# Kernel optimization log

Measured on AMD Instinct MI355X. Metric: run time of the kernel, lower is better.

Reference implementation:

```python
import jax, jax.numpy as jnp
import numpy as np
import jax.scipy.linalg as jsl

# ---- module constants (mirror __init__ buffers) ----
T0, T1, DT = 0.0, 1.0, 1e-3
DIM, NSTEPS, M, TQ, B = 8, 2048, 64, 1024, 1
DS = (T1 - T0) / NSTEPS
STEPS = jnp.linspace(T0, T1, NSTEPS + 1)            # [S+1]
ZPTS = jnp.linspace(T0 + DT * 5.5, T1 - DT * 5.5, M)  # inducing points [M]
SQRT_DS = float(np.sqrt(DS))
SQRT_DT = float(np.sqrt(DT))


def _hurst(t, y0, W1, b1, W2, b2, Wc1, bc1, Wc2, bc2, dw, cw):
    # compute_hurst: sigmoid(driving_action(t)*dw + condition_net(y0)*cw)
    tc_in = t.reshape(-1, 1)                                             # [N,1]
    feat = jnp.concatenate([jnp.sin(tc_in), jnp.cos(tc_in), tc_in], -1)  # [N,3]
    tc = jax.nn.sigmoid(jnp.tanh(feat @ W1.T + b1) @ W2.T + b2)          # [N,dim]
    pc = jax.nn.sigmoid(jnp.tanh(y0 @ Wc1.T + bc1) @ Wc2.T + bc2)        # [1,dim]
    return jax.nn.sigmoid(tc * dw + pc * cw)                             # [N,dim]


def _safe_pow(x, a):
    # x**a for x>=0, with well-defined (zero) gradient at x==0
    mask = x > 0
    xs = jnp.where(mask, x, 1.0)
    return jnp.where(mask, xs ** a, 0.0)


def _compute_weight(t, y0, params, eps=1e-12):
    # compute_weight (Muniandy et al. weight); returns [S, N, dim]
    h = _hurst(t, y0, *params)[None]                              # [1,N,dim]
    d0 = jax.nn.relu(t[None, :] - STEPS[:-1, None])[..., None]    # [S,N,1]
    d1 = jax.nn.relu(t[None, :] - STEPS[1:, None])[..., None]     # [S,N,1]
    w = jnp.sqrt(_safe_pow(d0, 2.0 * h) - _safe_pow(d1, 2.0 * h) + eps)
    w = w / jnp.sqrt(2.0 * h * DS)
    return w / jnp.exp(jax.lax.lgamma(h + 0.5))


def _increment_weight(t, y0, params):
    # increment_weight: g_i / dt (finite difference of clamped weights)
    wa = jnp.maximum(_compute_weight(t, y0, params), 0.0)
    wb = jnp.maximum(_compute_weight(t + DT, y0, params), 0.0)
    return jnp.maximum((wb - wa) * SQRT_DS / DT, 0.0)             # [S,N,dim]


def _forward(t, y0, eps_z, W1, b1, W2, b2, Wc1, bc1, Wc2, bc2, dw, cw):
    params = (W1, b1, W2, b2, Wc1, bc1, Wc2, bc2, dw, cw)
    # --- precompute (inducing points) ---
    Kz = _increment_weight(ZPTS, y0, params)                # [S,M,dim]
    Kzz = jnp.einsum('smd,skd->dmk', Kz, Kz)                # [dim,M,M]
    Lz = jnp.linalg.cholesky(Kzz + 1e-6 * jnp.eye(M, dtype=Kzz.dtype))
    delta_Bz = jnp.einsum('dmk,dkb->dmb', Lz, eps_z)        # [dim,M,B]
    # --- forward (mean / sqrt(var)*sqrt(dt)) ---
    Kt = _increment_weight(t, y0, params)                   # [S,T,dim]
    Ktz = jnp.einsum('std,smd->dtm', Kt, Kz)                # [dim,T,M]
    alpha = jax.vmap(lambda L, b: jsl.cho_solve((L, True), b))(
        Lz, jnp.swapaxes(Ktz, -1, -2))                      # [dim,M,T]
    mean = jnp.einsum('dmt,dmb->dtb', alpha, delta_Bz)      # [dim,T,B]
    Ktt = jnp.einsum('std,sud->dtu', Kt, Kt)                # [dim,T,T]
    var = Ktt - jnp.einsum('dmt,dmu->dtu', alpha, alpha)    # [dim,T,T]
    std = jnp.sqrt(jnp.maximum(var, 1e-12)) * SQRT_DT
    return mean.reshape(-1, DIM), std.reshape(-1, DIM)


def setup_inputs() -> dict:
    key = jax.random.key(0)
    ks = jax.random.split(key, 12)
    return {
        't': jax.random.uniform(ks[0], (TQ,), jnp.float32, T0 + 0.05, T1 - 0.05),
        'y0': jax.random.normal(ks[1], (1, 1), jnp.float32),
        'eps_z': jax.random.normal(ks[2], (DIM, M, B), jnp.float32),
        'W1': jax.random.normal(ks[3], (10, 3), jnp.float32) * 0.3,
        'b1': jax.random.normal(ks[4], (10,), jnp.float32) * 0.1,
        'W2': jax.random.normal(ks[5], (DIM, 10), jnp.float32) * 0.3,
        'b2': jax.random.normal(ks[6], (DIM,), jnp.float32) * 0.1,
        'Wc1': jax.random.normal(ks[7], (10, 1), jnp.float32) * 0.3,
        'bc1': jax.random.normal(ks[8], (10,), jnp.float32) * 0.1,
        'Wc2': jax.random.normal(ks[9], (DIM, 10), jnp.float32) * 0.3,
        'bc2': jax.random.normal(ks[10], (DIM,), jnp.float32) * 0.1,
        'dw': jnp.array([0.5], jnp.float32),
        'cw': jnp.array([0.5], jnp.float32),
    }


def reference(t, y0, eps_z, W1, b1, W2, b2, Wc1, bc1, Wc2, bc2, dw, cw):
    return _forward(t, y0, eps_z, W1, b1, W2, b2, Wc1, bc1, Wc2, bc2, dw, cw)
```

## Files before the change

### kernel.cpp

```cpp
#include <hip/hip_runtime.h>
#include <cmath>

#define DIMN 8
#define SSTEPS 2048
#define MZ 64
#define TQN 1024
#define DS_F    4.8828125e-4f
#define DT_F    1.0e-3f
#define SCALE_F 22.09708691207961f
#define SQRTDT_F 0.031622776601683794f
#define LN2_F   0.6931471805599453f

typedef _Float16 f16x8 __attribute__((ext_vector_type(8)));
typedef float f32x4 __attribute__((ext_vector_type(4)));

__device__ __forceinline__ float sigmoidf_(float x) { return 1.f / (1.f + expf(-x)); }

__device__ __forceinline__ void gl_lds16(const _Float16* g, _Float16* l)
{
    __builtin_amdgcn_global_load_lds(
        (const __attribute__((address_space(1))) unsigned int*)g,
        (__attribute__((address_space(3))) unsigned int*)l, 16, 0, 0);
}

__global__ void coef_kernel(const float* __restrict__ t_in, const float* __restrict__ y0,
                            const float* __restrict__ W1, const float* __restrict__ b1,
                            const float* __restrict__ W2, const float* __restrict__ b2,
                            const float* __restrict__ Wc1, const float* __restrict__ bc1,
                            const float* __restrict__ Wc2, const float* __restrict__ bc2,
                            const float* __restrict__ dw, const float* __restrict__ cw,
                            float4* __restrict__ coef_t, float4* __restrict__ coef_z,
                            float* __restrict__ times_z)
{
    int gid = blockIdx.x * blockDim.x + threadIdx.x;
    if (gid >= TQN + MZ) return;
    bool isz = gid >= TQN;
    float tv;
    if (!isz) {
        tv = t_in[gid];
    } else {
        int j = gid - TQN;
        tv = 0.0055f + (float)j * (0.989f / 63.0f);
        times_z[j] = tv;
    }
    float y = y0[0];
    float hc[10];
    #pragma unroll
    for (int j = 0; j < 10; ++j) hc[j] = tanhf(y * Wc1[j] + bc1[j]);
    float pc[DIMN];
    #pragma unroll
    for (int d = 0; d < DIMN; ++d) {
        float s = bc2[d];
        #pragma unroll
        for (int j = 0; j < 10; ++j) s += hc[j] * Wc2[d * 10 + j];
        pc[d] = sigmoidf_(s);
    }
    float dww = dw[0], cww = cw[0];
    float4 outv[DIMN];
    for (int which = 0; which < 2; ++which) {
        float tt = (which == 0) ? tv : tv + DT_F;
        float st = sinf(tt), ct = cosf(tt);
        float hid[10];
        #pragma unroll
        for (int j = 0; j < 10; ++j)
            hid[j] = tanhf(st * W1[j * 3 + 0] + ct * W1[j * 3 + 1] + tt * W1[j * 3 + 2] + b1[j]);
        #pragma unroll
        for (int d = 0; d < DIMN; ++d) {
            float s = b2[d];
            #pragma unroll
            for (int j = 0; j < 10; ++j) s += hid[j] * W2[d * 10 + j];
            float tc = sigmoidf_(s);
            float h = sigmoidf_(tc * dww + pc[d] * cww);
            float e = 2.f * h;
            float c = rsqrtf(e * DS_F) / tgammaf(h + 0.5f);
            if (which == 0) { outv[d].x = e; outv[d].y = c; }
            else            { outv[d].z = e; outv[d].w = c; }
        }
    }
    float4* dst = isz ? (coef_z + (size_t)(gid - TQN) * DIMN) : (coef_t + (size_t)gid * DIMN);
    #pragma unroll
    for (int d = 0; d < DIMN; ++d) dst[d] = outv[d];
}

__global__ __launch_bounds__(512) void sort_kernel(const float* __restrict__ t_in,
                                                   float* __restrict__ tsort,
                                                   int* __restrict__ perm,
                                                   int* __restrict__ inv)
{
    __shared__ float v[1024];
    __shared__ int   ix[1024];
    int tid = threadIdx.x;
    v[tid] = t_in[tid];             ix[tid] = tid;
    v[tid + 512] = t_in[tid + 512]; ix[tid + 512] = tid + 512;
    __syncthreads();
    for (int k = 2; k <= 1024; k <<= 1) {
        for (int j = k >> 1; j > 0; j >>= 1) {
            #pragma unroll 1
            for (int base = 0; base < 1024; base += 512) {
                int i = base + tid;
                int p = i ^ j;
                if (p > i) {
                    bool up = ((i & k) == 0);
                    float vi = v[i], vp = v[p];
                    if ((vi > vp) == up) {
                        v[i] = vp; v[p] = vi;
                        int q_ = ix[i]; ix[i] = ix[p]; ix[p] = q_;
                    }
                }
            }
            __syncthreads();
        }
    }
    tsort[tid] = v[tid];           tsort[tid + 512] = v[tid + 512];
    perm[tid] = ix[tid];           perm[tid + 512] = ix[tid + 512];
    inv[ix[tid]] = tid;            inv[ix[tid + 512]] = tid + 512;
}

__device__ __forceinline__ void side_weights(float tt, float e, float c, int sbase,
                                             float (&w)[8])
{
    float xprev = tt - (float)sbase * DS_F;
    float pa = 0.f;
    if (xprev > 0.f) pa = __builtin_amdgcn_exp2f(e * __builtin_amdgcn_logf(xprev));
    #pragma unroll
    for (int k = 1; k <= 8; ++k) {
        float xk = tt - (float)(sbase + k) * DS_F;
        float D, pan;
        if (xk > 0.f) {
            float om = xk * __builtin_amdgcn_rcpf(xprev);
            float y2 = e * __builtin_amdgcn_logf(om);
            float wl = y2 * LN2_F;
            float em = wl * (1.f + wl * (0.5f + wl * (0.16666667f + wl * (0.041666668f + wl * 0.008333334f))));
            float g = -em;
            if (wl < -0.3f) g = 1.f - __builtin_amdgcn_exp2f(y2);
            D = pa * g;
            pan = pa - D;
        } else {
            D = pa;
            pan = 0.f;
        }
        w[k - 1] = __builtin_amdgcn_sqrtf(D + 1e-12f) * c;
        pa = pan;
        xprev = xk;
    }
}

__device__ __forceinline__ unsigned pack_hl(float v)
{
    _Float16 h = (_Float16)v;
    _Float16 l = (_Float16)(v - (float)h);
    unsigned short hu = __builtin_bit_cast(unsigned short, h);
    unsigned short lu = __builtin_bit_cast(unsigned short, l);
    return (unsigned)hu | ((unsigned)lu << 16);
}

__global__ __launch_bounds__(256) void kmat_t_kernel(const float* __restrict__ tsort,
                                                     const int* __restrict__ perm,
                                                     const float4* __restrict__ coef,
                                                     _Float16* __restrict__ KThi,
                                                     _Float16* __restrict__ KTlo)
{
    int band = blockIdx.x >> 2;
    float bmax = tsort[band * 128 + 127];
    if ((float)(blockIdx.y * 64) * DS_F > bmax + DT_F + 0.07f) return;
    int tid = threadIdx.x;
    int txx = tid & 31, sidx = tid >> 5;
    int t = blockIdx.x * 32 + txx;
    int sbase = blockIdx.y * 64 + sidx * 8;
    int d = blockIdx.z;
    __shared__ unsigned shhl[32][65];
    float tq = tsort[t];
    float4 cf = coef[(size_t)perm[t] * DIMN + d];
    float wa[8], wb[8];
    side_weights(tq,        cf.x, cf.y, sbase, wa);
    side_weights(tq + DT_F, cf.z, cf.w, sbase, wb);
    #pragma unroll
    for (int k = 0; k < 8; ++k) {
        float v = fmaxf(wb[k] - wa[k], 0.f) * SCALE_F;
        shhl[txx][sidx * 8 + k] = pack_hl(v);
    }
    __syncthreads();
    int tl = tid >> 3, sc = tid & 7;
    unsigned dwv[8];
    #pragma unroll
    for (int j = 0; j < 8; ++j) dwv[j] = shhl[tl][sc * 8 + j];
    uint4 hv, lv;
    hv.x = __builtin_amdgcn_perm(dwv[1], dwv[0], 0x05040100u);
    hv.y = __builtin_amdgcn_perm(dwv[3], dwv[2], 0x05040100u);
    hv.z = __builtin_amdgcn_perm(dwv[5], dwv[4], 0x05040100u);
    hv.w = __builtin_amdgcn_perm(dwv[7], dwv[6], 0x05040100u);
    lv.x = __builtin_amdgcn_perm(dwv[1], dwv[0], 0x07060302u);
    lv.y = __builtin_amdgcn_perm(dwv[3], dwv[2], 0x07060302u);
    lv.z = __builtin_amdgcn_perm(dwv[5], dwv[4], 0x07060302u);
    lv.w = __builtin_amdgcn_perm(dwv[7], dwv[6], 0x07060302u);
    size_t o = ((size_t)(d * 1024) + blockIdx.x * 32 + tl) * 2048 + blockIdx.y * 64 + sc * 8;
    *(uint4*)&KThi[o] = hv;
    *(uint4*)&KTlo[o] = lv;
}

__global__ __launch_bounds__(256) void kmat_z_kernel(const float* __restrict__ times,
                                                     const float4* __restrict__ coef,
                                                     float* __restrict__ Kz,
                                                     _Float16* __restrict__ KzThi,
                                                     _Float16* __restrict__ KzTlo)
{
    int tid = threadIdx.x;
    int txx = tid & 31, sidx = tid >> 5;
    int m = blockIdx.x * 32 + txx;
    int sbase = blockIdx.y * 64 + sidx * 8;
    int d = blockIdx.z;
    __shared__ unsigned shhl[32][65];
    float tq = times[m];
    float4 cf = coef[(size_t)m * DIMN + d];
    float wa[8], wb[8];
    side_weights(tq,        cf.x, cf.y, sbase, wa);
    side_weights(tq + DT_F, cf.z, cf.w, sbase, wb);
    #pragma unroll
    for (int k = 0; k < 8; ++k) {
        float v = fmaxf(wb[k] - wa[k], 0.f) * SCALE_F;
        Kz[((size_t)d * SSTEPS + sbase + k) * 64 + m] = v;
        shhl[txx][sidx * 8 + k] = pack_hl(v);
    }
    __syncthreads();
    int tl = tid >> 3, sc = tid & 7;
    unsigned dwv[8];
    #pragma unroll
    for (int j = 0; j < 8; ++j) dwv[j] = shhl[tl][sc * 8 + j];
    uint4 hv, lv;
    hv.x = __builtin_amdgcn_perm(dwv[1], dwv[0], 0x05040100u);
    hv.y = __builtin_amdgcn_perm(dwv[3], dwv[2], 0x05040100u);
    hv.z = __builtin_amdgcn_perm(dwv[5], dwv[4], 0x05040100u);
    hv.w = __builtin_amdgcn_perm(dwv[7], dwv[6], 0x05040100u);
    lv.x = __builtin_amdgcn_perm(dwv[1], dwv[0], 0x07060302u);
    lv.y = __builtin_amdgcn_perm(dwv[3], dwv[2], 0x07060302u);
    lv.z = __builtin_amdgcn_perm(dwv[5], dwv[4], 0x07060302u);
    lv.w = __builtin_amdgcn_perm(dwv[7], dwv[6], 0x07060302u);
    size_t o = ((size_t)(d * 64) + blockIdx.x * 32 + tl) * 2048 + blockIdx.y * 64 + sc * 8;
    *(uint4*)&KzThi[o] = hv;
    *(uint4*)&KzTlo[o] = lv;
}

__global__ __launch_bounds__(256) void kzz_partial_kernel(const float* __restrict__ Kz,
                                                          float* __restrict__ part)
{
    int kidx = blockIdx.x;
    int d = blockIdx.y;
    int tid = threadIdx.x, tx = tid & 15, ty = tid >> 4;
    __shared__ float As[32][64];
    float acc[4][4] = {};
    const float* base = Kz + ((size_t)d * SSTEPS + (size_t)kidx * 256) * 64;
    for (int c = 0; c < 8; ++c) {
        __syncthreads();
        #pragma unroll
        for (int l = 0; l < 2; ++l) {
            int idx = tid + l * 256;
            int r = idx >> 4, c4 = idx & 15;
            *(float4*)&As[r][c4 * 4] = *(const float4*)(base + (size_t)(c * 32 + r) * 64 + c4 * 4);
        }
        __syncthreads();
        #pragma unroll
        for (int k = 0; k < 32; ++k) {
            float av[4], bv[4];
            *(float4*)&av[0] = *(float4*)&As[k][ty * 4];
            *(float4*)&bv[0] = *(float4*)&As[k][tx * 4];
            #pragma unroll
            for (int i = 0; i < 4; ++i)
                #pragma unroll
                for (int j = 0; j < 4; ++j) acc[i][j] += av[i] * bv[j];
        }
    }
    float* dst = part + (size_t)(kidx * DIMN + d) * 4096;
    #pragma unroll
    for (int i = 0; i < 4; ++i)
        *(float4*)&dst[(size_t)(ty * 4 + i) * 64 + tx * 4] =
            make_float4(acc[i][0], acc[i][1], acc[i][2], acc[i][3]);
}

__global__ void reduce_kernel(const float* __restrict__ in, float* __restrict__ out,
                              int n, int parts)
{
    int i = blockIdx.x * 256 + threadIdx.x;
    if (i >= n) return;
    float s = 0.f;
    for (int p = 0; p < parts; ++p) s += in[(size_t)p * n + i];
    out[i] = s;
}

__global__ __launch_bounds__(64) void chol_kernel(const float* __restrict__ Kzz,
                                                  const float* __restrict__ eps_z,
                                                  float* __restrict__ Lz, float* __restrict__ dBz)
{
    int d = blockIdx.x, i = threadIdx.x;
    __shared__ float A[64][65];
    for (int r = 0; r < 64; ++r)
        A[r][i] = Kzz[(size_t)d * 4096 + (size_t)r * 64 + i] + ((r == i) ? 1e-6f : 0.f);
    __syncthreads();
    for (int j = 0; j < 64; ++j) {
        float s = 0.f;
        if (i >= j) {
            float s0 = 0.f, s1 = 0.f, s2 = 0.f, s3 = 0.f;
            int k = 0;
            for (; k + 4 <= j; k += 4) {
                s0 += A[i][k]     * A[j][k];
                s1 += A[i][k + 1] * A[j][k + 1];
                s2 += A[i][k + 2] * A[j][k + 2];
                s3 += A[i][k + 3] * A[j][k + 3];
            }
            for (; k < j; ++k) s0 += A[i][k] * A[j][k];
            s = A[i][j] - ((s0 + s1) + (s2 + s3));
        }
        __syncthreads();
        if (i == j) A[j][j] = sqrtf(fmaxf(s, 1e-30f));
        __syncthreads();
        if (i > j) A[i][j] = s / A[j][j];
        __syncthreads();
    }
    for (int r = 0; r < 64; ++r)
        Lz[(size_t)d * 4096 + (size_t)r * 64 + i] = (i <= r) ? A[r][i] : 0.f;
    {
        float s0 = 0.f, s1 = 0.f, s2 = 0.f, s3 = 0.f;
        int k = 0;
        for (; k + 4 <= i + 1; k += 4) {
            s0 += A[i][k]     * eps_z[d * 64 + k];
            s1 += A[i][k + 1] * eps_z[d * 64 + k + 1];
            s2 += A[i][k + 2] * eps_z[d * 64 + k + 2];
            s3 += A[i][k + 3] * eps_z[d * 64 + k + 3];
        }
        for (; k <= i; ++k) s0 += A[i][k] * eps_z[d * 64 + k];
        dBz[d * 64 + i] = (s0 + s1) + (s2 + s3);
    }
}

__global__ __launch_bounds__(256, 2) void ktz_mfma_kernel(const _Float16* __restrict__ KThi,
                                                          const _Float16* __restrict__ KTlo,
                                                          const _Float16* __restrict__ KzThi,
                                                          const _Float16* __restrict__ KzTlo,
                                                          const float* __restrict__ tsort,
                                                          float* __restrict__ part)
{
    int tid = threadIdx.x;
    int wave = tid >> 6, lane = tid & 63;
    int n = lane & 15, q = lane >> 4;
    int lr = lane >> 2, lc = (lane & 3) * 8;
    int d = blockIdx.x;
    int t0 = blockIdx.y * 128;
    int split = blockIdx.z;
    int wr = (wave >> 1) * 64, wc = (wave & 1) * 32;

    float tmax = tsort[t0 + 127];
    int klim = (int)floorf((tmax + DT_F) * 64.f) + 2;
    int nc = klim - split * 16;
    nc = nc < 0 ? 0 : (nc > 16 ? 16 : nc);

    __shared__ _Float16 Ah[2][128][32], Al[2][128][32];
    __shared__ _Float16 Bh[2][64][32],  Bl[2][64][32];

    f32x4 acc[4][2];
    #pragma unroll
    for (int i = 0; i < 4; ++i)
        #pragma unroll
        for (int j = 0; j < 2; ++j) acc[i][j] = (f32x4)0.f;

    const size_t aRow = (size_t)(d * 1024 + t0);
    const size_t bRow = (size_t)(d * 64);
    int segA = wave * 32;
    int segB = wave * 16;

    auto stage = [&](int buf, int c) {
        int s0 = split * 512 + c * 32;
        size_t ga = (aRow + segA + lr) * 2048 + s0 + lc;
        size_t gb = (bRow + segB + lr) * 2048 + s0 + lc;
        gl_lds16(KThi + ga,               &Ah[buf][segA][0]);
        gl_lds16(KThi + ga + 16 * 2048,   &Ah[buf][segA + 16][0]);
        gl_lds16(KTlo + ga,               &Al[buf][segA][0]);
        gl_lds16(KTlo + ga + 16 * 2048,   &Al[buf][segA + 16][0]);
        gl_lds16(KzThi + gb,              &Bh[buf][segB][0]);
        gl_lds16(KzTlo + gb,              &Bl[buf][segB][0]);
    };

    if (nc > 0) stage(0, 0);
    for (int c = 0; c < nc; ++c) {
        int buf = c & 1;
        asm volatile("s_waitcnt vmcnt(0)" ::: "memory");
        __builtin_amdgcn_s_barrier();
        __builtin_amdgcn_sched_barrier(0);
        if (c + 1 < nc) stage(buf ^ 1, c + 1);
        f16x8 fAh[4], fAl[4], fBh[2], fBl[2];
        #pragma unroll
        for (int i = 0; i < 4; ++i) {
            fAh[i] = *(f16x8*)&Ah[buf][wr + i * 16 + n][q * 8];
            fAl[i] = *(f16x8*)&Al[buf][wr + i * 16 + n][q * 8];
        }
        #pragma unroll
        for (int j = 0; j < 2; ++j) {
            fBh[j] = *(f16x8*)&Bh[buf][wc + j * 16 + n][q * 8];
            fBl[j] = *(f16x8*)&Bl[buf][wc + j * 16 + n][q * 8];
        }
        __builtin_amdgcn_s_setprio(1);
        #pragma unroll
        for (int i = 0; i < 4; ++i)
            #pragma unroll
            for (int j = 0; j < 2; ++j) {
                acc[i][j] = __builtin_amdgcn_mfma_f32_16x16x32_f16(fAh[i], fBh[j], acc[i][j], 0, 0, 0);
                acc[i][j] = __builtin_amdgcn_mfma_f32_16x16x32_f16(fAh[i], fBl[j], acc[i][j], 0, 0, 0);
                acc[i][j] = __builtin_amdgcn_mfma_f32_16x16x32_f16(fAl[i], fBh[j], acc[i][j], 0, 0, 0);
            }
        __builtin_amdgcn_s_setprio(0);
    }
    float* dst = part + ((size_t)(split * DIMN + d)) * 1024 * 64;
    #pragma unroll
    for (int i = 0; i < 4; ++i)
        #pragma unroll
        for (int j = 0; j < 2; ++j)
            #pragma unroll
            for (int r = 0; r < 4; ++r) {
                int t = t0 + wr + i * 16 + q * 4 + r;
                dst[(size_t)t * 64 + wc + j * 16 + n] = acc[i][j][r];
            }
}

__global__ __launch_bounds__(64) void solve_kernel(const float* __restrict__ Lz,
                                                   const float* __restrict__ part2,
                                                   const float* __restrict__ dBz,
                                                   const int* __restrict__ perm,
                                                   _Float16* __restrict__ aPhi,
                                                   _Float16* __restrict__ aPlo,
                                                   _Float16* __restrict__ aNhi,
                                                   _Float16* __restrict__ aNlo,
                                                   float* __restrict__ out0)
{
    int d = blockIdx.y;
    int t0 = blockIdx.x * 64;
    int i = threadIdx.x;
    __shared__ float L[64][68];
    __shared__ float LT[64][68];
    __shared__ float bLs[64][65];
    __shared__ float inv[64];
    __shared__ float dB[64];
    for (int r = 0; r < 64; ++r) {
        float v = Lz[(size_t)d * 4096 + (size_t)r * 64 + i];
        L[r][i] = v;
        LT[i][r] = v;
    }
    dB[i] = dBz[d * 64 + i];
    for (int r = 0; r < 64; ++r) {
        size_t base = ((size_t)d * 1024 + t0 + r) * 64 + i;
        bLs[i][r] = (part2[base] + part2[base + 524288]) +
                    (part2[base + 1048576] + part2[base + 1572864]);
    }
    __syncthreads();
    inv[i] = 1.f / L[i][i];
    __syncthreads();
    float x[64];
    #pragma unroll
    for (int k = 0; k < 64; ++k) x[k] = bLs[k][i];
    #pragma unroll
    for (int j = 0; j < 64; ++j) {
        float s0 = 0.f, s1 = 0.f, s2 = 0.f, s3 = 0.f;
        #pragma unroll
        for (int k = 0; k + 4 <= j; k += 4) {
            float4 lv = *(const float4*)&L[j][k];
            s0 += lv.x * x[k];     s1 += lv.y * x[k + 1];
            s2 += lv.z * x[k + 2]; s3 += lv.w * x[k + 3];
        }
        #pragma unroll
        for (int k = j & ~3; k < j; ++k) s0 += L[j][k] * x[k];
        x[j] = (x[j] - ((s0 + s1) + (s2 + s3))) * inv[j];
    }
    #pragma unroll
    for (int j = 63; j >= 0; --j) {
        float s0 = 0.f, s1 = 0.f, s2 = 0.f, s3 = 0.f;
        #pragma unroll
        for (int k = j + 1; k < ((j + 4) & ~3); ++k) s0 += LT[j][k] * x[k];
        #pragma unroll
        for (int k = (j + 4) & ~3; k + 4 <= 64; k += 4) {
            float4 lv = *(const float4*)&LT[j][k];
            s0 += lv.x * x[k];     s1 += lv.y * x[k + 1];
            s2 += lv.z * x[k + 2]; s3 += lv.w * x[k + 3];
        }
        x[j] = (x[j] - ((s0 + s1) + (s2 + s3))) * inv[j];
    }
    {
        float m0 = 0.f, m1 = 0.f, m2 = 0.f, m3 = 0.f;
        #pragma unroll
        for (int m = 0; m < 64; m += 4) {
            m0 += x[m]     * dB[m];
            m1 += x[m + 1] * dB[m + 1];
            m2 += x[m + 2] * dB[m + 2];
            m3 += x[m + 3] * dB[m + 3];
        }
        out0[d * 1024 + perm[t0 + i]] = (m0 + m1) + (m2 + m3);
    }
    size_t o = ((size_t)(d * 1024 + t0 + i)) * 64;
    #pragma unroll
    for (int g = 0; g < 8; ++g) {
        union { _Float16 h[8]; float4 v; } ph, pl, nh, nl;
        #pragma unroll
        for (int k = 0; k < 8; ++k) {
            float xv = x[g * 8 + k];
            _Float16 h = (_Float16)xv;
            _Float16 lo = (_Float16)(xv - (float)h);
            ph.h[k] = h;  pl.h[k] = lo;
            nh.h[k] = -h; nl.h[k] = -lo;
        }
        *(float4*)&aPhi[o + g * 8] = ph.v;
        *(float4*)&aPlo[o + g * 8] = pl.v;
        *(float4*)&aNhi[o + g * 8] = nh.v;
        *(float4*)&aNlo[o + g * 8] = nl.v;
    }
}

__global__ __launch_bounds__(256, 3) void var_mfma_kernel(const _Float16* __restrict__ KThi,
                                                          const _Float16* __restrict__ KTlo,
                                                          const _Float16* __restrict__ aPhi,
                                                          const _Float16* __restrict__ aPlo,
                                                          const _Float16* __restrict__ aNhi,
                                                          const _Float16* __restrict__ aNlo,
                                                          const float* __restrict__ tsort,
                                                          const int* __restrict__ perm,
                                                          float* __restrict__ out1)
{
    int tid = threadIdx.x;
    int wave = tid >> 6, lane = tid & 63;
    int n = lane & 15, q = lane >> 4;
    int lr = lane >> 2;
    int lcs = (((lane & 3) ^ ((lr >> 1) & 3)) * 8);
    int qs  = ((q ^ ((n >> 1) & 3)) * 8);
    int d = blockIdx.x;
    int ti = 0, rem = blockIdx.y;
    while (rem >= 16 - 2 * ti) { rem -= 16 - 2 * ti; ++ti; }
    int uj = 2 * ti + rem;
    int t0 = ti * 128, u0 = uj * 64;
    int wr = (wave >> 1) * 64, wc = (wave & 1) * 32;

    float tmaxv = tsort[t0 + 127];
    float umaxv = tsort[u0 + 63];
    int nck = (int)floorf((fminf(tmaxv, umaxv) + DT_F) * 64.f) + 2;
    if (nck > 64) nck = 64;
    int nit = nck + 2;

    __shared__ _Float16 Ah[2][128][32], Al[2][128][32];
    __shared__ _Float16 Bh[2][64][32],  Bl[2][64][32];

    f32x4 acc[4][2];
    #pragma unroll
    for (int i = 0; i < 4; ++i)
        #pragma unroll
        for (int j = 0; j < 2; ++j) acc[i][j] = (f32x4)0.f;

    const size_t aRow = (size_t)(d * 1024 + t0);
    const size_t bRow = (size_t)(d * 1024 + u0);
    int sa = wave * 32;
    int sb = wave * 16;

    auto stage = [&](int buf, int ck) {
        const _Float16 *ph, *pl, *qh, *ql;
        size_t str; int col;
        if (ck < 64) { ph = KThi; pl = KTlo; qh = KThi; ql = KTlo; str = 2048; col = ck * 32; }
        else         { ph = aPhi; pl = aPlo; qh = aNhi; ql = aNlo; str = 64;  col = (ck - 64) * 32; }
        size_t ga = (aRow + sa + lr) * str + col + lcs;
        size_t gb = (bRow + sb + lr) * str + col + lcs;
        gl_lds16(ph + ga,            &Ah[buf][sa][0]);
        gl_lds16(ph + ga + 16 * str, &Ah[buf][sa + 16][0]);
        gl_lds16(pl + ga,            &Al[buf][sa][0]);
        gl_lds16(pl + ga + 16 * str, &Al[buf][sa + 16][0]);
        gl_lds16(qh + gb,            &Bh[buf][sb][0]);
        gl_lds16(ql + gb,            &Bl[buf][sb][0]);
    };

    stage(0, 0);
    for (int it = 0; it < nit; ++it) {
        int buf = it & 1;
        asm volatile("s_waitcnt vmcnt(0)" ::: "memory");
        __builtin_amdgcn_s_barrier();
        __builtin_amdgcn_sched_barrier(0);
        int nx = it + 1;
        if (nx < nit) stage(buf ^ 1, nx < nck ? nx : 64 + (nx - nck));
        f16x8 fAh[4], fAl[4], fBh[2], fBl[2];
        #pragma unroll
        for (int i = 0; i < 4; ++i) {
            fAh[i] = *(f16x8*)&Ah[buf][wr + i * 16 + n][qs];
            fAl[i] = *(f16x8*)&Al[buf][wr + i * 16 + n][qs];
        }
        #pragma unroll
        for (int j = 0; j < 2; ++j) {
            fBh[j] = *(f16x8*)&Bh[buf][wc + j * 16 + n][qs];
            fBl[j] = *(f16x8*)&Bl[buf][wc + j * 16 + n][qs];
        }
        __builtin_amdgcn_s_setprio(1);
        #pragma unroll
        for (int i = 0; i < 4; ++i)
            #pragma unroll
            for (int j = 0; j < 2; ++j) {
                acc[i][j] = __builtin_amdgcn_mfma_f32_16x16x32_f16(fAh[i], fBh[j], acc[i][j], 0, 0, 0);
                acc[i][j] = __builtin_amdgcn_mfma_f32_16x16x32_f16(fAh[i], fBl[j], acc[i][j], 0, 0, 0);
                acc[i][j] = __builtin_amdgcn_mfma_f32_16x16x32_f16(fAl[i], fBh[j], acc[i][j], 0, 0, 0);
            }
        __builtin_amdgcn_s_setprio(0);
    }
    float* dst = out1 + ((size_t)d << 20);
    int tw0 = t0 + wr;
    int uw0 = u0 + wc;
    bool above = (uw0 >= tw0 + 64);
    bool below = (uw0 + 32 <= tw0);
    if (!below) {
        #pragma unroll
        for (int i = 0; i < 4; ++i) {
            int tb = tw0 + i * 16 + q * 4;
            #pragma unroll
            for (int j = 0; j < 2; ++j) {
                int u = uw0 + j * 16 + n;
                int pu = perm[u];
                float fv[4];
                #pragma unroll
                for (int r = 0; r < 4; ++r)
                    fv[r] = sqrtf(fmaxf(acc[i][j][r], 1e-12f)) * SQRTDT_F;
                if (above) {
                    #pragma unroll
                    for (int r = 0; r < 4; ++r)
                        dst[(size_t)perm[tb + r] * 1024 + u] = fv[r];
                    *(float4*)&dst[(size_t)pu * 1024 + tb] = make_float4(fv[0], fv[1], fv[2], fv[3]);
                } else {
                    #pragma unroll
                    for (int r = 0; r < 4; ++r) {
                        int t = tb + r;
                        if (u >= t) dst[(size_t)perm[t] * 1024 + u] = fv[r];
                        if (u > t)  dst[(size_t)pu * 1024 + t] = fv[r];
                    }
                }
            }
        }
    }
}

__global__ __launch_bounds__(256) void colperm_kernel(float* __restrict__ out1,
                                                      const int* __restrict__ invp)
{
    int d = blockIdx.y, row = blockIdx.x;
    float* rp = out1 + ((size_t)d << 20) + (size_t)row * 1024;
    __shared__ float buf[1024];
    int tid = threadIdx.x;
    *(float4*)&buf[tid * 4] = *(float4*)&rp[tid * 4];
    __syncthreads();
    #pragma unroll
    for (int k = 0; k < 4; ++k) {
        int b = tid + k * 256;
        rp[b] = buf[invp[b]];
    }
}

extern "C" void kernel_launch(void* const* d_in, const int* in_sizes, int n_in,
                              void* d_out, int out_size, void* d_ws, size_t ws_size,
                              hipStream_t stream)
{
    const float* t_in  = (const float*)d_in[0];
    const float* y0    = (const float*)d_in[1];
    const float* eps_z = (const float*)d_in[2];
    const float* W1    = (const float*)d_in[3];
    const float* b1    = (const float*)d_in[4];
    const float* W2    = (const float*)d_in[5];
    const float* b2    = (const float*)d_in[6];
    const float* Wc1   = (const float*)d_in[7];
    const float* bc1   = (const float*)d_in[8];
    const float* Wc2   = (const float*)d_in[9];
    const float* bc2   = (const float*)d_in[10];
    const float* dw    = (const float*)d_in[11];
    const float* cw    = (const float*)d_in[12];

    float* ws = (float*)d_ws;
    size_t off = 0;
    auto carve = [&](size_t n) { float* p = ws + off; off += n; return p; };
    float* coef_t   = carve(32768);
    float* coef_z   = carve(2048);
    float* times_z  = carve(64);
    float* Kzz      = carve(32768);
    float* Lz       = carve(32768);
    float* dBz      = carve(512);
    float* Kz       = carve(1048576);
    _Float16* KThi  = (_Float16*)carve(8388608);
    _Float16* KTlo  = (_Float16*)carve(8388608);
    _Float16* KzThi = (_Float16*)carve(524288);
    _Float16* KzTlo = (_Float16*)carve(524288);
    float* part1    = carve(262144);
    float* part2    = carve(2097152);
    _Float16* aPhi  = (_Float16*)carve(262144);
    _Float16* aPlo  = (_Float16*)carve(262144);
    _Float16* aNhi  = (_Float16*)carve(262144);
    _Float16* aNlo  = (_Float16*)carve(262144);
    float* tsort    = carve(1024);
    int*   perm_i   = (int*)carve(1024);
    int*   inv_i    = (int*)carve(1024);

    float* out0 = (float*)d_out;
    float* out1 = out0 + (size_t)DIMN * 1024;

    coef_kernel<<<9, 128, 0, stream>>>(t_in, y0, W1, b1, W2, b2, Wc1, bc1, Wc2, bc2, dw, cw,
                                       (float4*)coef_t, (float4*)coef_z, times_z);
    sort_kernel<<<1, 512, 0, stream>>>(t_in, tsort, perm_i, inv_i);
    kmat_t_kernel<<<dim3(32, 32, 8), 256, 0, stream>>>(tsort, perm_i, (const float4*)coef_t,
                                                       KThi, KTlo);
    kmat_z_kernel<<<dim3(2, 32, 8), 256, 0, stream>>>(times_z, (const float4*)coef_z,
                                                      Kz, KzThi, KzTlo);
    kzz_partial_kernel<<<dim3(8, 8), 256, 0, stream>>>(Kz, part1);
    reduce_kernel<<<128, 256, 0, stream>>>(part1, Kzz, 32768, 8);
    chol_kernel<<<8, 64, 0, stream>>>(Kzz, eps_z, Lz, dBz);
    ktz_mfma_kernel<<<dim3(8, 8, 4), 256, 0, stream>>>(KThi, KTlo, KzThi, KzTlo, tsort, part2);
    solve_kernel<<<dim3(16, 8), 64, 0, stream>>>(Lz, part2, dBz, perm_i,
                                                 aPhi, aPlo, aNhi, aNlo, out0);
    var_mfma_kernel<<<dim3(8, 72), 256, 0, stream>>>(KThi, KTlo, aPhi, aPlo, aNhi, aNlo,
                                                     tsort, perm_i, out1);
    colperm_kernel<<<dim3(1024, 8), 256, 0, stream>>>(out1, inv_i);
}
```

Baseline: 357.4 us.

## Rewrite Cholesky as register-resident right-looking update with wave shuffles

The 64x64 Cholesky per dimension moves from a left-looking LDS dot-product loop with three barriers per column to a right-looking update. Each lane holds its row in registers and column values are broadcast with wave shuffles, so no barriers are needed inside the loop. The eps_z product is accumulated on the fly, which removes the separate triangular matvec. The cost is many shuffles (about 2000 per lane across the unrolled loop) and 64 registers per lane for the row.

After: 340.7 us. -4.7%, faster.

```diff
diff --git a/kernel.cpp b/kernel.cpp
--- a/kernel.cpp
+++ b/kernel.cpp
@@ -295,40 +295,26 @@
     for (int r = 0; r < 64; ++r)
         A[r][i] = Kzz[(size_t)d * 4096 + (size_t)r * 64 + i] + ((r == i) ? 1e-6f : 0.f);
     __syncthreads();
+    float a[64];
+    #pragma unroll
+    for (int k = 0; k < 64; ++k) a[k] = A[i][k];
+    float veps = eps_z[d * 64 + i];
+    float db = 0.f;
+    #pragma unroll
     for (int j = 0; j < 64; ++j) {
-        float s = 0.f;
-        if (i >= j) {
-            float s0 = 0.f, s1 = 0.f, s2 = 0.f, s3 = 0.f;
-            int k = 0;
-            for (; k + 4 <= j; k += 4) {
-                s0 += A[i][k]     * A[j][k];
-                s1 += A[i][k + 1] * A[j][k + 1];
-                s2 += A[i][k + 2] * A[j][k + 2];
-                s3 += A[i][k + 3] * A[j][k + 3];
-            }
-            for (; k < j; ++k) s0 += A[i][k] * A[j][k];
-            s = A[i][j] - ((s0 + s1) + (s2 + s3));
-        }
-        __syncthreads();
-        if (i == j) A[j][j] = sqrtf(fmaxf(s, 1e-30f));
-        __syncthreads();
-        if (i > j) A[i][j] = s / A[j][j];
-        __syncthreads();
-    }
+        float dsq = __shfl(a[j], j);
+        float dj = sqrtf(fmaxf(dsq, 1e-30f));
+        float l = (i >= j) ? (a[j] / dj) : 0.f;
+        A[i][j] = l;
+        db += l * __shfl(veps, j);
+        #pragma unroll
+        for (int k = j + 1; k < 64; ++k)
+            a[k] -= l * __shfl(l, k);
+    }
+    __syncthreads();
     for (int r = 0; r < 64; ++r)
         Lz[(size_t)d * 4096 + (size_t)r * 64 + i] = (i <= r) ? A[r][i] : 0.f;
-    {
-        float s0 = 0.f, s1 = 0.f, s2 = 0.f, s3 = 0.f;
-        int k = 0;
-        for (; k + 4 <= i + 1; k += 4) {
-            s0 += A[i][k]     * eps_z[d * 64 + k];
-            s1 += A[i][k + 1] * eps_z[d * 64 + k + 1];
-            s2 += A[i][k + 2] * eps_z[d * 64 + k + 2];
-            s3 += A[i][k + 3] * eps_z[d * 64 + k + 3];
-        }
-        for (; k <= i; ++k) s0 += A[i][k] * eps_z[d * 64 + k];
-        dBz[d * 64 + i] = (s0 + s1) + (s2 + s3);
-    }
+    dBz[d * 64 + i] = db;
 }
 
 __global__ __launch_bounds__(256, 2) void ktz_mfma_kernel(const _Float16* __restrict__ KThi,
```
